# Kernel optimization log

Hardware: AMD Instinct MI355X
Metric: run time of the kernel (lower is better)

The kernel has to match this reference:

```python
import jax, jax.numpy as jnp
import numpy as np

# Static sensor configuration (from init_kwargs)
WIDTH = 1024
HEIGHT = 1024
X0, Y0 = -1.0, -1.0
DX = (1.0 - (-1.0)) / WIDTH
DY = (1.0 - (-1.0)) / HEIGHT
SIGMA = 0.1
KERNEL_SIZE = 2

_off = np.arange(-KERNEL_SIZE, KERNEL_SIZE + 1)
_ox, _oy = np.meshgrid(_off, _off, indexing='xy')
OFF_X = jnp.asarray(_ox.flatten(), dtype=jnp.int32)  # [(2k+1)^2] = [25]
OFF_Y = jnp.asarray(_oy.flatten(), dtype=jnp.int32)

N_POINTS = 2_000_000


def setup_inputs() -> dict:
    key = jax.random.key(0)
    k1, k2, k3 = jax.random.split(key, 3)
    x = jax.random.uniform(k1, (N_POINTS,), dtype=jnp.float32)       # in [0,1) subset of bounds
    y = jax.random.uniform(k2, (N_POINTS,), dtype=jnp.float32)
    values = jax.random.normal(k3, (N_POINTS,), dtype=jnp.float32)
    return {"x": x, "y": y, "values": values}


def reference(x, y, values):
    # Map to pixel coordinates
    x_pix = (x - X0) / DX
    y_pix = (y - Y0) / DY
    xi_base = jnp.floor(x_pix).astype(jnp.int32)
    yi_base = jnp.floor(y_pix).astype(jnp.int32)
    x_frac = x_pix - xi_base
    y_frac = y_pix - yi_base

    # [N, 25] neighbor pixel indices and Gaussian weights
    xi = xi_base[:, None] + OFF_X[None, :]
    yi = yi_base[:, None] + OFF_Y[None, :]
    dist_x = x_frac[:, None] - OFF_X[None, :].astype(x_frac.dtype)
    dist_y = y_frac[:, None] - OFF_Y[None, :].astype(y_frac.dtype)
    weights = jnp.exp(-0.5 * (dist_x ** 2 + dist_y ** 2) / (SIGMA ** 2))
    weights = weights / jnp.sum(weights, axis=1, keepdims=True)

    valid = (xi >= 0) & (xi < WIDTH) & (yi >= 0) & (yi < HEIGHT)
    xi = jnp.clip(xi, 0, WIDTH - 1)
    yi = jnp.clip(yi, 0, HEIGHT - 1)

    splatted = values[:, None] * weights * valid  # [N, 25]
    flat_idx = (yi * WIDTH + xi).reshape(-1)      # [N*25]
    img_flat = jax.ops.segment_sum(splatted.reshape(-1), flat_idx,
                                   num_segments=HEIGHT * WIDTH)
    return img_flat.reshape(HEIGHT, WIDTH)
```

## Files before the change

kernel.cpp:

```cpp
#include <hip/hip_runtime.h>
#include <hip/hip_bf16.h>

#define WIDTH 1024
#define HEIGHT 1024
#define IMG_ELEMS (WIDTH * HEIGHT)
#define TPX 32
#define NTILES (TPX * TPX)
#define NB 256
#define BT 1024
#define CAPR 80
#define CAPP 36
#define PTS_CAP 8448


__device__ __forceinline__ void point_geom(float px, float py, int& cxb, int& cyb,
                                           float& ax, float& ay) {
    float xp = (px + 1.0f) * 512.0f;
    float yp = (py + 1.0f) * 512.0f;
    int xb = (int)floorf(xp);
    int yb = (int)floorf(yp);
    float xf = xp - (float)xb;
    float yf = yp - (float)yb;
    float wx0 = __expf(-50.0f * xf * xf);
    float wx1 = __expf(-50.0f * (1.0f - xf) * (1.0f - xf));
    float wy0 = __expf(-50.0f * yf * yf);
    float wy1 = __expf(-50.0f * (1.0f - yf) * (1.0f - yf));
    ax = wx0 / (wx0 + wx1);
    ay = wy0 / (wy0 + wy1);
    cxb = min(max(xb, 0), WIDTH - 1);
    cyb = min(max(yb, 0), HEIGHT - 1);
}

__global__ void __launch_bounds__(BT)
k_sortlocal(const float* __restrict__ x, const float* __restrict__ y,
            const float* __restrict__ v, uint2* __restrict__ payload,
            unsigned* __restrict__ runCnt, int n, int ppb) {
    __shared__ unsigned cursor[NTILES];
    int b = blockIdx.x;
    for (int t = threadIdx.x; t < NTILES; t += BT) cursor[t] = 0u;
    __syncthreads();
    int lo = b * ppb;
    int hi = min(n, lo + ppb);
    for (int i = lo + threadIdx.x; i < hi; i += BT) {
        int cxb, cyb; float ax, ay;
        point_geom(x[i], y[i], cxb, cyb, ax, ay);
        int tile = (cyb >> 5) * TPX + (cxb >> 5);
        unsigned pos = atomicAdd(&cursor[tile], 1u);
        if (pos < CAPR) {
            unsigned axq = (unsigned)(ax * 2047.0f + 0.5f);
            unsigned ayq = (unsigned)(ay * 2047.0f + 0.5f);
            unsigned packed = axq | (ayq << 11) |
                              ((unsigned)(cxb & 31) << 22) | ((unsigned)(cyb & 31) << 27);
            payload[(size_t)((unsigned)(b << 10) | (unsigned)tile) * CAPR + pos] =
                make_uint2(__float_as_uint(v[i]), packed);
        }
    }
    __syncthreads();
    for (int t = threadIdx.x; t < NTILES; t += BT)
        runCnt[t * NB + b] = min(cursor[t], (unsigned)CAPR);
}

__global__ void __launch_bounds__(BT)
k_totals(const unsigned* __restrict__ runCnt, unsigned* __restrict__ tileTotal) {
    int t = blockIdx.x * 16 + (threadIdx.x >> 6);
    int lane = threadIdx.x & 63;
    unsigned s = 0u;
#pragma unroll
    for (int k = 0; k < 4; ++k) s += runCnt[t * NB + k * 64 + lane];
#pragma unroll
    for (int d = 32; d >= 1; d >>= 1) s += __shfl_down(s, d, 64);
    if (lane == 0) tileTotal[t] = s;
}

__global__ void __launch_bounds__(NTILES)
k_worklist(const unsigned* __restrict__ tileTotal, unsigned* __restrict__ worklist,
           unsigned* __restrict__ nActive) {
    __shared__ unsigned nact, ninact;
    int t = threadIdx.x;
    if (t == 0) { nact = 0u; ninact = 0u; }
    __syncthreads();
    unsigned c = tileTotal[t];
    if (c) worklist[atomicAdd(&nact, 1u)] = (unsigned)t;
    else   worklist[NTILES - 1u - atomicAdd(&ninact, 1u)] = (unsigned)t;
    __syncthreads();
    if (t == 0) nActive[0] = nact;
}

__global__ void __launch_bounds__(BT)
k_accum(const uint2* __restrict__ payload, const unsigned* __restrict__ runCnt,
        const unsigned* __restrict__ worklist, const unsigned* __restrict__ nActive,
        float* __restrict__ t00p, float* __restrict__ t10p,
        float* __restrict__ t01p, float* __restrict__ t11p) {
    __shared__ uint2 pts[PTS_CAP];
    __shared__ unsigned short bidx[NTILES * CAPP];
    __shared__ unsigned hcnt[NTILES];
    __shared__ unsigned rcnt[NB], rdst[NB], stmp[NB];
    unsigned b = blockIdx.x;
    unsigned nA = nActive[0];
    int p = threadIdx.x;
    int lx = p & 31, ly = p >> 5;

    if (b >= nA) {
        unsigned t = worklist[NTILES - 1u - (b - nA)];
        int gx = (int)((t & 31u) << 5) + lx;
        int gy = (int)((t >> 5) << 5) + ly;
        size_t idx = (size_t)gy * WIDTH + gx;
        t00p[idx] = 0.0f; t10p[idx] = 0.0f; t01p[idx] = 0.0f; t11p[idx] = 0.0f;
        return;
    }

    unsigned t = worklist[b];
    if (p < NB) { unsigned c = runCnt[t * NB + p]; rcnt[p] = c; stmp[p] = c; }
    hcnt[p] = 0u;
    __syncthreads();
    for (int d = 1; d < NB; d <<= 1) {
        unsigned add = 0u;
        if (p < NB && p >= d) add = stmp[p - d];
        __syncthreads();
        if (p < NB) stmp[p] += add;
        __syncthreads();
    }
    if (p < NB) rdst[p] = stmp[p] - rcnt[p];
    __syncthreads();

    int w = p >> 6, lane = p & 63;
    for (int k = 0; k < 16; ++k) {
        int r = w * 16 + k;
        unsigned cnt = rcnt[r], dst = rdst[r];
        const uint2* g = payload + (size_t)((unsigned)(r << 10) | t) * CAPR;
        for (unsigned j = lane; j < cnt; j += 64) {
            uint2 pl = g[j];
            unsigned slot = dst + j;
            if (slot < PTS_CAP) {
                pts[slot] = pl;
                unsigned pix = (pl.y >> 22) & 1023u;
                unsigned pos = atomicAdd(&hcnt[pix], 1u);
                if (pos < CAPP) bidx[pix * CAPP + pos] = (unsigned short)slot;
            }
        }
    }
    __syncthreads();

    float t00 = 0.0f, t10 = 0.0f, t01 = 0.0f, t11 = 0.0f;
    unsigned cnt = min(hcnt[p], (unsigned)CAPP);
    for (unsigned e = 0; e < cnt; ++e) {
        uint2 sp = pts[bidx[p * CAPP + e]];
        float val = __uint_as_float(sp.x);
        float ax = (float)(sp.y & 2047u) * (1.0f / 2047.0f);
        float ay = (float)((sp.y >> 11) & 2047u) * (1.0f / 2047.0f);
        float bx = 1.0f - ax, by = 1.0f - ay;
        t00 += val * ax * ay;
        t10 += val * bx * ay;
        t01 += val * ax * by;
        t11 += val * bx * by;
    }
    int gx = (int)((t & 31u) << 5) + lx;
    int gy = (int)((t >> 5) << 5) + ly;
    size_t idx = (size_t)gy * WIDTH + gx;
    t00p[idx] = t00; t10p[idx] = t10; t01p[idx] = t01; t11p[idx] = t11;
}

__global__ void __launch_bounds__(256)
k_merge(const float* __restrict__ t00p, const float* __restrict__ t10p,
        const float* __restrict__ t01p, const float* __restrict__ t11p,
        float* __restrict__ out) {
    int i = blockIdx.x * 256 + threadIdx.x;
    int xx = i & (WIDTH - 1);
    int yy = i >> 10;
    float val = t00p[i];
    if (xx > 0)           val += t10p[i - 1];
    if (yy > 0)           val += t01p[i - WIDTH];
    if (xx > 0 && yy > 0) val += t11p[i - WIDTH - 1];
    out[i] = val;
}

__global__ void __launch_bounds__(256)
splat_direct(const float* __restrict__ x, const float* __restrict__ y,
             const float* __restrict__ v, float* __restrict__ out, int n) {
    int i = blockIdx.x * blockDim.x + threadIdx.x;
    if (i >= n) return;
    int cxb, cyb; float ax, ay;
    point_geom(x[i], y[i], cxb, cyb, ax, ay);
    float val = v[i];
    float bx = 1.0f - ax, by = 1.0f - ay;
    float* row = out + cyb * WIDTH;
    atomicAdd(row + cxb, val * ax * ay);
    if (cxb + 1 < WIDTH) atomicAdd(row + cxb + 1, val * bx * ay);
    if (cyb + 1 < HEIGHT) {
        row += WIDTH;
        atomicAdd(row + cxb, val * ax * by);
        if (cxb + 1 < WIDTH) atomicAdd(row + cxb + 1, val * bx * by);
    }
}

extern "C" void kernel_launch(void* const* d_in, const int* in_sizes, int n_in,
                              void* d_out, int out_size, void* d_ws, size_t ws_size,
                              hipStream_t stream) {
    const float* x = (const float*)d_in[0];
    const float* y = (const float*)d_in[1];
    const float* v = (const float*)d_in[2];
    float* out = (float*)d_out;
    int n = in_sizes[0];
    int ppb = (n + NB - 1) / NB;

    size_t off_payload = 0;
    size_t off_planes  = off_payload + (size_t)NB * NTILES * CAPR * sizeof(uint2);
    size_t off_runcnt  = off_planes + 4ull * IMG_ELEMS * sizeof(float);
    size_t off_total   = off_runcnt + (size_t)NTILES * NB * sizeof(unsigned);
    size_t off_wl      = off_total + 4096;
    size_t off_nact    = off_wl + 4096;
    size_t need        = off_nact + 4096;

    bool caps_ok = (ppb <= 8192);

    if (ws_size >= need && caps_ok) {
        char* ws = (char*)d_ws;
        uint2*    payload   = (uint2*)(ws + off_payload);
        float*    t00p      = (float*)(ws + off_planes);
        float*    t10p      = t00p + IMG_ELEMS;
        float*    t01p      = t10p + IMG_ELEMS;
        float*    t11p      = t01p + IMG_ELEMS;
        unsigned* runCnt    = (unsigned*)(ws + off_runcnt);
        unsigned* tileTotal = (unsigned*)(ws + off_total);
        unsigned* worklist  = (unsigned*)(ws + off_wl);
        unsigned* nActive   = (unsigned*)(ws + off_nact);

        k_sortlocal<<<NB, BT, 0, stream>>>(x, y, v, payload, runCnt, n, ppb);
        k_totals<<<64, BT, 0, stream>>>(runCnt, tileTotal);
        k_worklist<<<1, NTILES, 0, stream>>>(tileTotal, worklist, nActive);
        k_accum<<<NTILES, BT, 0, stream>>>(payload, runCnt, worklist, nActive,
                                           t00p, t10p, t01p, t11p);
        k_merge<<<IMG_ELEMS / 256, 256, 0, stream>>>(t00p, t10p, t01p, t11p, out);
    } else {
        hipMemsetAsync(out, 0, (size_t)out_size * sizeof(float), stream);
        splat_direct<<<(n + 255) / 256, 256, 0, stream>>>(x, y, v, out, n);
    }
}
```

Baseline: 109.2 us.

## Fuse tile totals, worklist and merge into accumulation kernel with halo atomics

Drops the totals, worklist and merge kernels and the four intermediate image planes. Each accumulation block now sums its own run counts with wave shuffles, exits early if its tile is empty, and does the 2x2 neighbour merge in shared memory. Contributions that cross a tile border go to the output with atomics after a memset. A hardcoded block-to-tile order schedules the populated quadrant (x,y in [0,1) maps to tiles 16-31) first, replacing the dynamic worklist. This removes launches and plane traffic, but adds a memset, atomics at tile edges, and a schedule that assumes the input distribution.

```diff
diff --git a/kernel.cpp b/kernel.cpp
--- a/kernel.cpp
+++ b/kernel.cpp
@@ -11,6 +11,14 @@
 #define CAPR 80
 #define CAPP 36
 #define PTS_CAP 8448
+
+#define OFF_PTS   0
+#define OFF_BIDX  (OFF_PTS + 2 * PTS_CAP)
+#define OFF_HCNT  (OFF_BIDX + (NTILES * CAPP) / 2)
+#define OFF_RCNT  (OFF_HCNT + NTILES)
+#define OFF_RDST  (OFF_RCNT + NB)
+#define OFF_STMP  (OFF_RDST + NB)
+#define SMEM_U32  (OFF_STMP + NB)
 
 
 __device__ __forceinline__ void point_geom(float px, float py, int& cxb, int& cyb,
@@ -37,7 +45,7 @@
             unsigned* __restrict__ runCnt, int n, int ppb) {
     __shared__ unsigned cursor[NTILES];
     int b = blockIdx.x;
-    for (int t = threadIdx.x; t < NTILES; t += BT) cursor[t] = 0u;
+    cursor[threadIdx.x] = 0u;
     __syncthreads();
     int lo = b * ppb;
     int hi = min(n, lo + ppb);
@@ -56,76 +64,65 @@
         }
     }
     __syncthreads();
-    for (int t = threadIdx.x; t < NTILES; t += BT)
-        runCnt[t * NB + b] = min(cursor[t], (unsigned)CAPR);
-}
-
-__global__ void __launch_bounds__(BT)
-k_totals(const unsigned* __restrict__ runCnt, unsigned* __restrict__ tileTotal) {
-    int t = blockIdx.x * 16 + (threadIdx.x >> 6);
-    int lane = threadIdx.x & 63;
-    unsigned s = 0u;
-#pragma unroll
-    for (int k = 0; k < 4; ++k) s += runCnt[t * NB + k * 64 + lane];
-#pragma unroll
-    for (int d = 32; d >= 1; d >>= 1) s += __shfl_down(s, d, 64);
-    if (lane == 0) tileTotal[t] = s;
-}
-
-__global__ void __launch_bounds__(NTILES)
-k_worklist(const unsigned* __restrict__ tileTotal, unsigned* __restrict__ worklist,
-           unsigned* __restrict__ nActive) {
-    __shared__ unsigned nact, ninact;
-    int t = threadIdx.x;
-    if (t == 0) { nact = 0u; ninact = 0u; }
-    __syncthreads();
-    unsigned c = tileTotal[t];
-    if (c) worklist[atomicAdd(&nact, 1u)] = (unsigned)t;
-    else   worklist[NTILES - 1u - atomicAdd(&ninact, 1u)] = (unsigned)t;
-    __syncthreads();
-    if (t == 0) nActive[0] = nact;
+    runCnt[threadIdx.x * NB + b] = min(cursor[threadIdx.x], (unsigned)CAPR);
 }
 
 __global__ void __launch_bounds__(BT)
 k_accum(const uint2* __restrict__ payload, const unsigned* __restrict__ runCnt,
-        const unsigned* __restrict__ worklist, const unsigned* __restrict__ nActive,
-        float* __restrict__ t00p, float* __restrict__ t10p,
-        float* __restrict__ t01p, float* __restrict__ t11p) {
-    __shared__ uint2 pts[PTS_CAP];
-    __shared__ unsigned short bidx[NTILES * CAPP];
-    __shared__ unsigned hcnt[NTILES];
-    __shared__ unsigned rcnt[NB], rdst[NB], stmp[NB];
+        float* __restrict__ out) {
+    __shared__ unsigned smem[SMEM_U32];
+    uint2*          pts  = (uint2*)&smem[OFF_PTS];
+    unsigned short* bidx = (unsigned short*)&smem[OFF_BIDX];
+    unsigned*       hcnt = &smem[OFF_HCNT];
+    unsigned*       rcnt = &smem[OFF_RCNT];
+    unsigned*       rdst = &smem[OFF_RDST];
+    unsigned*       stmp = &smem[OFF_STMP];
+    float*          exT01 = (float*)&smem[OFF_PTS];
+    float*          exT11 = (float*)&smem[OFF_PTS + BT];
+
     unsigned b = blockIdx.x;
-    unsigned nA = nActive[0];
+    unsigned t;
+    if (b < 256u) {
+        t = (16u + (b >> 4)) * 32u + 16u + (b & 15u);
+    } else {
+        unsigned r = b - 256u;
+        if (r < 512u) t = r;
+        else { unsigned q = r - 512u; t = (16u + (q >> 4)) * 32u + (q & 15u); }
+    }
+
     int p = threadIdx.x;
-    int lx = p & 31, ly = p >> 5;
-
-    if (b >= nA) {
-        unsigned t = worklist[NTILES - 1u - (b - nA)];
-        int gx = (int)((t & 31u) << 5) + lx;
-        int gy = (int)((t >> 5) << 5) + ly;
-        size_t idx = (size_t)gy * WIDTH + gx;
-        t00p[idx] = 0.0f; t10p[idx] = 0.0f; t01p[idx] = 0.0f; t11p[idx] = 0.0f;
-        return;
-    }
-
-    unsigned t = worklist[b];
-    if (p < NB) { unsigned c = runCnt[t * NB + p]; rcnt[p] = c; stmp[p] = c; }
+    unsigned lane = p & 63, w = p >> 6;
+    unsigned c0 = 0u;
+    if (p < NB) { c0 = runCnt[t * NB + p]; rcnt[p] = c0; }
     hcnt[p] = 0u;
-    __syncthreads();
-    for (int d = 1; d < NB; d <<= 1) {
-        unsigned add = 0u;
-        if (p < NB && p >= d) add = stmp[p - d];
-        __syncthreads();
-        if (p < NB) stmp[p] += add;
-        __syncthreads();
-    }
-    if (p < NB) rdst[p] = stmp[p] - rcnt[p];
-    __syncthreads();
-
-    int w = p >> 6, lane = p & 63;
+    unsigned tsum = c0;
+#pragma unroll
+    for (int d = 32; d >= 1; d >>= 1) tsum += __shfl_down(tsum, d, 64);
+    if (p < NB && lane == 0) rdst[w] = tsum;
+    __syncthreads();
+    unsigned total = rdst[0] + rdst[1] + rdst[2] + rdst[3];
+    if (total == 0) return;
+
+    unsigned vsc = c0;
+#pragma unroll
+    for (int d = 1; d < 64; d <<= 1) {
+        unsigned tmp = __shfl_up(vsc, d, 64);
+        if (lane >= (unsigned)d) vsc += tmp;
+    }
+    __syncthreads();
+    if (p < NB && lane == 63) stmp[w] = vsc;
+    __syncthreads();
+    if (p == 0) {
+        unsigned a = 0;
+#pragma unroll
+        for (int k = 0; k < 4; ++k) { unsigned tt = stmp[k]; stmp[k] = a; a += tt; }
+    }
+    __syncthreads();
+    if (p < NB) rdst[p] = vsc - c0 + stmp[w];
+    __syncthreads();
+
     for (int k = 0; k < 16; ++k) {
-        int r = w * 16 + k;
+        int r = (int)w * 16 + k;
         unsigned cnt = rcnt[r], dst = rdst[r];
         const uint2* g = payload + (size_t)((unsigned)(r << 10) | t) * CAPR;
         for (unsigned j = lane; j < cnt; j += 64) {
@@ -154,24 +151,32 @@
         t01 += val * ax * by;
         t11 += val * bx * by;
     }
+    __syncthreads();
+    exT01[p] = t01;
+    exT11[p] = t11;
+    __syncthreads();
+
+    int lx = p & 31, ly = p >> 5;
     int gx = (int)((t & 31u) << 5) + lx;
     int gy = (int)((t >> 5) << 5) + ly;
-    size_t idx = (size_t)gy * WIDTH + gx;
-    t00p[idx] = t00; t10p[idx] = t10; t01p[idx] = t01; t11p[idx] = t11;
-}
-
-__global__ void __launch_bounds__(256)
-k_merge(const float* __restrict__ t00p, const float* __restrict__ t10p,
-        const float* __restrict__ t01p, const float* __restrict__ t11p,
-        float* __restrict__ out) {
-    int i = blockIdx.x * 256 + threadIdx.x;
-    int xx = i & (WIDTH - 1);
-    int yy = i >> 10;
-    float val = t00p[i];
-    if (xx > 0)           val += t10p[i - 1];
-    if (yy > 0)           val += t01p[i - WIDTH];
-    if (xx > 0 && yy > 0) val += t11p[i - WIDTH - 1];
-    out[i] = val;
+    size_t g = (size_t)gy * WIDTH + gx;
+    float t10l = __shfl_up(t10, 1, 64);
+    float sum = t00;
+    if (lx > 0) sum += t10l;
+    if (ly > 0) sum += exT01[p - 32];
+    if (lx > 0 && ly > 0) sum += exT11[p - 33];
+    if (lx == 0 || ly == 0) atomicAdd(&out[g], sum);
+    else out[g] = sum;
+
+    bool xr = (gx + 1 < WIDTH), yd = (gy + 1 < HEIGHT);
+    if (lx == 31 && xr) {
+        atomicAdd(&out[g + 1], t10);
+        if (yd) atomicAdd(&out[g + WIDTH + 1], t11);
+    }
+    if (ly == 31 && yd) {
+        atomicAdd(&out[g + WIDTH], t01);
+        if (lx < 31 && xr) atomicAdd(&out[g + WIDTH + 1], t11);
+    }
 }
 
 __global__ void __launch_bounds__(256)
@@ -204,33 +209,18 @@
     int ppb = (n + NB - 1) / NB;
 
     size_t off_payload = 0;
-    size_t off_planes  = off_payload + (size_t)NB * NTILES * CAPR * sizeof(uint2);
-    size_t off_runcnt  = off_planes + 4ull * IMG_ELEMS * sizeof(float);
-    size_t off_total   = off_runcnt + (size_t)NTILES * NB * sizeof(unsigned);
-    size_t off_wl      = off_total + 4096;
-    size_t off_nact    = off_wl + 4096;
-    size_t need        = off_nact + 4096;
-
+    size_t off_runcnt  = off_payload + (size_t)NB * NTILES * CAPR * sizeof(uint2);
+    size_t need        = off_runcnt + (size_t)NTILES * NB * sizeof(unsigned);
     bool caps_ok = (ppb <= 8192);
 
     if (ws_size >= need && caps_ok) {
         char* ws = (char*)d_ws;
-        uint2*    payload   = (uint2*)(ws + off_payload);
-        float*    t00p      = (float*)(ws + off_planes);
-        float*    t10p      = t00p + IMG_ELEMS;
-        float*    t01p      = t10p + IMG_ELEMS;
-        float*    t11p      = t01p + IMG_ELEMS;
-        unsigned* runCnt    = (unsigned*)(ws + off_runcnt);
-        unsigned* tileTotal = (unsigned*)(ws + off_total);
-        unsigned* worklist  = (unsigned*)(ws + off_wl);
-        unsigned* nActive   = (unsigned*)(ws + off_nact);
-
+        uint2*    payload = (uint2*)(ws + off_payload);
+        unsigned* runCnt  = (unsigned*)(ws + off_runcnt);
+
+        hipMemsetAsync(out, 0, (size_t)out_size * sizeof(float), stream);
         k_sortlocal<<<NB, BT, 0, stream>>>(x, y, v, payload, runCnt, n, ppb);
-        k_totals<<<64, BT, 0, stream>>>(runCnt, tileTotal);
-        k_worklist<<<1, NTILES, 0, stream>>>(tileTotal, worklist, nActive);
-        k_accum<<<NTILES, BT, 0, stream>>>(payload, runCnt, worklist, nActive,
-                                           t00p, t10p, t01p, t11p);
-        k_merge<<<IMG_ELEMS / 256, 256, 0, stream>>>(t00p, t10p, t01p, t11p, out);
+        k_accum<<<NTILES, BT, 0, stream>>>(payload, runCnt, out);
     } else {
         hipMemsetAsync(out, 0, (size_t)out_size * sizeof(float), stream);
         splat_direct<<<(n + 255) / 256, 256, 0, stream>>>(x, y, v, out, n);
```

Measured after the change: 104.7 us. -4.1%, faster.
